# Optimization experiments

Hardware: AMD Instinct MI355X
Metric: run time of the kernel (lower is better)

## Reference

```python
import jax, jax.numpy as jnp
import numpy as np

N = 50000        # nodes
E = 100000       # directed edges
F_NODE = 22      # atom features
F_EDGE = 4       # bond features
H = 64           # hidden_dim
EPS = 1e-5       # BatchNorm eps


def setup_inputs() -> dict:
    key = jax.random.key(0)
    ks = jax.random.split(key, 16)
    s = 0.05
    return {
        "x": jax.random.normal(ks[0], (N, F_NODE), dtype=jnp.float32),
        "edge_attr": jax.random.normal(ks[1], (E, F_EDGE), dtype=jnp.float32),
        "We1": jax.random.normal(ks[2], (F_EDGE, F_NODE * H), dtype=jnp.float32) * s,
        "be1": jnp.zeros((F_NODE * H,), dtype=jnp.float32),
        "root1": jax.random.normal(ks[3], (F_NODE, H), dtype=jnp.float32) * s,
        "b1": jnp.zeros((H,), dtype=jnp.float32),
        "g1": jnp.ones((H,), dtype=jnp.float32),
        "beta1": jnp.zeros((H,), dtype=jnp.float32),
        "We2": jax.random.normal(ks[4], (F_EDGE, H * H), dtype=jnp.float32) * s,
        "be2": jnp.zeros((H * H,), dtype=jnp.float32),
        "root2": jax.random.normal(ks[5], (H, H), dtype=jnp.float32) * s,
        "b2": jnp.zeros((H,), dtype=jnp.float32),
        "g2": jnp.ones((H,), dtype=jnp.float32),
        "beta2": jnp.zeros((H,), dtype=jnp.float32),
        "Wfc": jax.random.normal(ks[6], (H, 1), dtype=jnp.float32) * s,
        "bfc": jnp.zeros((1,), dtype=jnp.float32),
        "edge_index": jax.random.randint(ks[7], (2, E), 0, N, dtype=jnp.int32),
    }


def nnconv(x, edge_index, edge_attr, We, be, root, bias, in_ch, out_ch):
    # PyG NNConv (aggr='add', root_weight=True):
    #   out_i = x_i @ root + bias + sum_{(j->i)} x_j @ reshape(MLP(e_ji), [in, out])
    src, dst = edge_index[0], edge_index[1]
    w = jax.nn.relu(edge_attr @ We + be).reshape(-1, in_ch, out_ch)  # [E, in, out]
    msg = jnp.einsum('ei,eio->eo', x[src], w)                        # [E, out]
    agg = jax.ops.segment_sum(msg, dst, num_segments=x.shape[0])     # [N, out]
    return agg + x @ root + bias


def batchnorm(x, gamma, beta):
    # training-mode BatchNorm1d: batch statistics, biased variance
    mu = jnp.mean(x, axis=0)
    var = jnp.mean(jnp.square(x - mu), axis=0)
    return (x - mu) * jax.lax.rsqrt(var + EPS) * gamma + beta


def reference(x, edge_attr, We1, be1, root1, b1, g1, beta1,
              We2, be2, root2, b2, g2, beta2, Wfc, bfc, edge_index):
    h = nnconv(x, edge_index, edge_attr, We1, be1, root1, b1, F_NODE, H)
    h = jax.nn.relu(batchnorm(h, g1, beta1))
    # dropout is identity in eval / deterministic reference
    h = nnconv(h, edge_index, edge_attr, We2, be2, root2, b2, H, H)
    h = jax.nn.relu(batchnorm(h, g2, beta2))
    return jax.nn.sigmoid(h @ Wfc + bfc)  # [N, 1]
```

## Files before the change

### kernel.cpp

```cpp
#include <hip/hip_runtime.h>
#include <math.h>

#define N_NODES 50000
#define N_EDGES 100000
#define FNODE 22
#define HDIM 64
#define BN_EPS 1e-5f

typedef __attribute__((ext_vector_type(8))) short bfrag;
typedef __attribute__((ext_vector_type(4))) float facc;
typedef __attribute__((ext_vector_type(4))) unsigned int uint4v;
typedef __attribute__((ext_vector_type(2))) unsigned int uint2v;

__device__ __forceinline__ unsigned f2bf(float x) {
    unsigned u = __float_as_uint(x);
    return (u + 0x7FFFu + ((u >> 16) & 1u)) >> 16;
}
__device__ __forceinline__ unsigned pk2bf(float lo, float hi) {
    return f2bf(lo) | (f2bf(hi) << 16);
}
__device__ __forceinline__ float bflo(unsigned w) { return __uint_as_float(w << 16); }
__device__ __forceinline__ float bfhi(unsigned w) { return __uint_as_float(w & 0xFFFF0000u); }

__global__ void k_packX(const float* __restrict__ x, unsigned* __restrict__ xbf) {
    int idx = blockIdx.x * 256 + threadIdx.x;
    if (idx < N_NODES * 12) {
        int n = idx / 12, c2 = idx - n * 12;
        int c = c2 * 2;
        float lo = (c < FNODE) ? x[n * FNODE + c] : 0.f;
        float hi = (c + 1 < FNODE) ? x[n * FNODE + c + 1] : 0.f;
        xbf[idx] = pk2bf(lo, hi);
    }
}

template <int K>
__global__ void k_packB(const float* __restrict__ W, uint4v* __restrict__ Bt) {
    constexpr int NQ = (K + 31) / 32;
    int t = threadIdx.x;
    int ot = t >> 6, lane = t & 63;
    int o = ot * 16 + (lane & 15);
    int kg = lane >> 4;
#pragma unroll
    for (int q = 0; q < NQ; ++q) {
        unsigned w[4];
#pragma unroll
        for (int p = 0; p < 4; ++p) {
            int k0 = q * 32 + kg * 8 + 2 * p;
            float lo = (k0 < K) ? W[k0 * HDIM + o] : 0.f;
            float hi = (k0 + 1 < K) ? W[(k0 + 1) * HDIM + o] : 0.f;
            w[p] = pk2bf(lo, hi);
        }
        Bt[(ot * NQ + q) * 64 + lane] = uint4v{w[0], w[1], w[2], w[3]};
    }
}

__global__ void k_node1(const float* __restrict__ x, const uint4v* __restrict__ Bt1,
                        const float* __restrict__ b1, float* __restrict__ h1) {
    int lane = threadIdx.x & 63;
    int m = lane & 15, kg = lane >> 4, orow4 = kg * 4;
    int tile = blockIdx.x * 4 + (threadIdx.x >> 6);
    int nb = tile * 16;
    if (nb >= N_NODES) return;
    const float* xr = x + (size_t)(nb + m) * FNODE;
    float xv[8];
#pragma unroll
    for (int p = 0; p < 4; ++p) {
        int c = kg * 8 + 2 * p;
        float2 v = (c + 1 < FNODE) ? *(const float2*)(xr + c) : float2{0.f, 0.f};
        xv[2 * p] = v.x; xv[2 * p + 1] = v.y;
    }
    bfrag A = __builtin_bit_cast(bfrag, uint4v{pk2bf(xv[0], xv[1]), pk2bf(xv[2], xv[3]),
                                               pk2bf(xv[4], xv[5]), pk2bf(xv[6], xv[7])});
    const facc zero4 = {0.f, 0.f, 0.f, 0.f};
#pragma unroll
    for (int ot = 0; ot < 4; ++ot) {
        bfrag B = __builtin_bit_cast(bfrag, Bt1[ot * 64 + lane]);
        facc d = __builtin_amdgcn_mfma_f32_16x16x32_bf16(A, B, zero4, 0, 0, 0);
        float bv = b1[ot * 16 + m];
#pragma unroll
        for (int j = 0; j < 4; ++j)
            h1[(size_t)(nb + orow4 + j) * HDIM + ot * 16 + m] = d[j] + bv;
    }
}

template <int IN, int ROWB, int SSTRIDE, int MINW>
__launch_bounds__(256, MINW)
__global__ void k_edge(const char* __restrict__ hrows, const float* __restrict__ ea,
                       const float* __restrict__ We, const float* __restrict__ be,
                       const int* __restrict__ eidx, float* __restrict__ out) {
    constexpr int INH = IN * HDIM;
    __shared__ uint4v Wf[IN * 32];
    __shared__ unsigned hsl[4][32 * SSTRIDE];

    int obeg = (blockIdx.x & 1) * 32;
    int tileblk = blockIdx.x >> 1;

    for (int idx = threadIdx.x; idx < IN * 32; idx += 256) {
        int i = idx >> 5, oloc = idx & 31;
        int c = i * HDIM + obeg + oloc;
        Wf[idx] = uint4v{pk2bf(We[c], We[INH + c]),
                         pk2bf(We[2 * INH + c], We[3 * INH + c]),
                         f2bf(be[c]), 0u};
    }
    __syncthreads();

    int lane = threadIdx.x & 63;
    int e16 = lane & 15;
    int orow4 = (lane >> 4) * 4;
    int tile = tileblk * 4 + (threadIdx.x >> 6);
    int ebase = tile * 32;
    if (ebase >= N_EDGES) return;
    unsigned* hs = &hsl[threadIdx.x >> 6][0];

    bool act = lane < 16;
    float4 ea0 = ((const float4*)ea)[ebase + e16];
    float4 ea1 = ((const float4*)ea)[ebase + 16 + e16];
    unsigned aone = act ? 0x3F80u : 0u;
    bfrag A0 = __builtin_bit_cast(bfrag, uint4v{act ? pk2bf(ea0.x, ea0.y) : 0u,
                                                act ? pk2bf(ea0.z, ea0.w) : 0u, aone, 0u});
    bfrag A1 = __builtin_bit_cast(bfrag, uint4v{act ? pk2bf(ea1.x, ea1.y) : 0u,
                                                act ? pk2bf(ea1.z, ea1.w) : 0u, aone, 0u});

    constexpr int SPR = ROWB / 16;
    constexpr int SLOTS = 32 * SPR;
#pragma unroll
    for (int p = 0; p < (SLOTS + 63) / 64; ++p) {
        int idx = p * 64 + lane;
        if ((SLOTS % 64 == 0) || idx < SLOTS) {
            int r = idx / SPR, c16 = idx - r * SPR;
            int src = eidx[ebase + r];
            uint4v hv = *(const uint4v*)(hrows + (size_t)src * ROWB + c16 * 16);
            *(uint4v*)&hs[r * SSTRIDE + c16 * 4] = hv;
        }
    }

    const facc zero4 = {0.f, 0.f, 0.f, 0.f};
    facc m0[2] = {zero4, zero4}, m1[2] = {zero4, zero4};

    constexpr int I4 = IN & ~3;
#pragma unroll
    for (int i0 = 0; i0 < I4; i0 += 4) {
        float hA[4][4], hB[4][4];
#pragma unroll
        for (int j = 0; j < 4; ++j) {
            uint2v wA = *(const uint2v*)&hs[(orow4 + j) * SSTRIDE + i0 / 2];
            hA[j][0] = bflo(wA.x); hA[j][1] = bfhi(wA.x);
            hA[j][2] = bflo(wA.y); hA[j][3] = bfhi(wA.y);
            uint2v wB = *(const uint2v*)&hs[(16 + orow4 + j) * SSTRIDE + i0 / 2];
            hB[j][0] = bflo(wB.x); hB[j][1] = bfhi(wB.x);
            hB[j][2] = bflo(wB.y); hB[j][3] = bfhi(wB.y);
        }
#pragma unroll
        for (int di = 0; di < 4; ++di) {
#pragma unroll
            for (int t = 0; t < 2; ++t) {
                bfrag B = __builtin_bit_cast(bfrag, Wf[(i0 + di) * 32 + t * 16 + e16]);
                facc t0 = __builtin_amdgcn_mfma_f32_16x16x32_bf16(A0, B, zero4, 0, 0, 0);
                facc t1 = __builtin_amdgcn_mfma_f32_16x16x32_bf16(A1, B, zero4, 0, 0, 0);
#pragma unroll
                for (int j = 0; j < 4; ++j) {
                    m0[t][j] = fmaf(hA[j][di], fmaxf(t0[j], 0.f), m0[t][j]);
                    m1[t][j] = fmaf(hB[j][di], fmaxf(t1[j], 0.f), m1[t][j]);
                }
            }
        }
    }
    if constexpr ((IN & 3) != 0) {
        float hA[4][2], hB[4][2];
#pragma unroll
        for (int j = 0; j < 4; ++j) {
            unsigned wA = hs[(orow4 + j) * SSTRIDE + I4 / 2];
            hA[j][0] = bflo(wA); hA[j][1] = bfhi(wA);
            unsigned wB = hs[(16 + orow4 + j) * SSTRIDE + I4 / 2];
            hB[j][0] = bflo(wB); hB[j][1] = bfhi(wB);
        }
#pragma unroll
        for (int di = 0; di < (IN & 3); ++di) {
#pragma unroll
            for (int t = 0; t < 2; ++t) {
                bfrag B = __builtin_bit_cast(bfrag, Wf[(I4 + di) * 32 + t * 16 + e16]);
                facc t0 = __builtin_amdgcn_mfma_f32_16x16x32_bf16(A0, B, zero4, 0, 0, 0);
                facc t1 = __builtin_amdgcn_mfma_f32_16x16x32_bf16(A1, B, zero4, 0, 0, 0);
#pragma unroll
                for (int j = 0; j < 4; ++j) {
                    m0[t][j] = fmaf(hA[j][di], fmaxf(t0[j], 0.f), m0[t][j]);
                    m1[t][j] = fmaf(hB[j][di], fmaxf(t1[j], 0.f), m1[t][j]);
                }
            }
        }
    }

    int dA[4], dB[4];
#pragma unroll
    for (int j = 0; j < 4; ++j) {
        dA[j] = eidx[N_EDGES + ebase + orow4 + j];
        dB[j] = eidx[N_EDGES + ebase + 16 + orow4 + j];
    }
#pragma unroll
    for (int t = 0; t < 2; ++t) {
#pragma unroll
        for (int j = 0; j < 4; ++j) {
            atomicAdd(&out[(size_t)dA[j] * HDIM + obeg + t * 16 + e16], m0[t][j]);
            atomicAdd(&out[(size_t)dB[j] * HDIM + obeg + t * 16 + e16], m1[t][j]);
        }
    }
}

__global__ void k_stats(const float* __restrict__ hbuf, float* stats) {
    int c = threadIdx.x & 63;
    int r = threadIdx.x >> 6;
    int rowsPer = blockDim.x >> 6;
    float s = 0.f, q = 0.f;
    for (int n = blockIdx.x * rowsPer + r; n < N_NODES; n += gridDim.x * rowsPer) {
        float v = hbuf[n * HDIM + c];
        s += v;
        q = fmaf(v, v, q);
    }
    __shared__ float ls[4][64], lq[4][64];
    ls[r][c] = s;
    lq[r][c] = q;
    __syncthreads();
    if (r == 0) {
        s = ls[0][c] + ls[1][c] + ls[2][c] + ls[3][c];
        q = lq[0][c] + lq[1][c] + lq[2][c] + lq[3][c];
        atomicAdd(&stats[c], s);
        atomicAdd(&stats[64 + c], q);
    }
}

__global__ void k_finalize(const float* stats_in, const float* __restrict__ g,
                           const float* __restrict__ beta, float* as_out) {
    int c = threadIdx.x;
    float mu = stats_in[c] * (1.f / N_NODES);
    float var = stats_in[64 + c] * (1.f / N_NODES) - mu * mu;
    var = fmaxf(var, 0.f);
    float a = g[c] * rsqrtf(var + BN_EPS);
    as_out[c] = a;
    as_out[64 + c] = beta[c] - mu * a;
}

__global__ void k_apply1(const float* h1, const float* __restrict__ as1,
                         const uint4v* __restrict__ Bt, const float* __restrict__ b2,
                         unsigned* __restrict__ hbf, float* h2) {
    int lane = threadIdx.x & 63;
    int m = lane & 15, kg = lane >> 4, orow4 = (lane >> 4) * 4;
    int tile = blockIdx.x * 4 + (threadIdx.x >> 6);
    int nb = tile * 16;
    if (nb >= N_NODES) return;
    int node = nb + m;
    const float* hr = h1 + (size_t)node * HDIM;

    float4 a0 = *(const float4*)(as1 + kg * 8), a1 = *(const float4*)(as1 + kg * 8 + 4);
    float4 s0 = *(const float4*)(as1 + 64 + kg * 8), s1 = *(const float4*)(as1 + 64 + kg * 8 + 4);
    float4 a2 = *(const float4*)(as1 + 32 + kg * 8), a3 = *(const float4*)(as1 + 32 + kg * 8 + 4);
    float4 s2 = *(const float4*)(as1 + 96 + kg * 8), s3 = *(const float4*)(as1 + 96 + kg * 8 + 4);

    float4 v0 = *(const float4*)(hr + kg * 8), v1 = *(const float4*)(hr + kg * 8 + 4);
    float4 v2 = *(const float4*)(hr + 32 + kg * 8), v3 = *(const float4*)(hr + 32 + kg * 8 + 4);

    float r0[8], r1[8];
#pragma unroll
    for (int p = 0; p < 4; ++p) {
        r0[p]     = fmaxf(fmaf((&v0.x)[p], (&a0.x)[p], (&s0.x)[p]), 0.f);
        r0[p + 4] = fmaxf(fmaf((&v1.x)[p], (&a1.x)[p], (&s1.x)[p]), 0.f);
        r1[p]     = fmaxf(fmaf((&v2.x)[p], (&a2.x)[p], (&s2.x)[p]), 0.f);
        r1[p + 4] = fmaxf(fmaf((&v3.x)[p], (&a3.x)[p], (&s3.x)[p]), 0.f);
    }
    uint4v pk0 = uint4v{pk2bf(r0[0], r0[1]), pk2bf(r0[2], r0[3]),
                        pk2bf(r0[4], r0[5]), pk2bf(r0[6], r0[7])};
    uint4v pk1 = uint4v{pk2bf(r1[0], r1[1]), pk2bf(r1[2], r1[3]),
                        pk2bf(r1[4], r1[5]), pk2bf(r1[6], r1[7])};
    *(uint4v*)(hbf + (size_t)node * 32 + kg * 4)      = pk0;
    *(uint4v*)(hbf + (size_t)node * 32 + 16 + kg * 4) = pk1;

    bfrag A0 = __builtin_bit_cast(bfrag, pk0);
    bfrag A1 = __builtin_bit_cast(bfrag, pk1);

    const facc zero4 = {0.f, 0.f, 0.f, 0.f};
#pragma unroll
    for (int ot = 0; ot < 4; ++ot) {
        bfrag B0 = __builtin_bit_cast(bfrag, Bt[(ot * 2 + 0) * 64 + lane]);
        bfrag B1 = __builtin_bit_cast(bfrag, Bt[(ot * 2 + 1) * 64 + lane]);
        facc d = __builtin_amdgcn_mfma_f32_16x16x32_bf16(A0, B0, zero4, 0, 0, 0);
        d = __builtin_amdgcn_mfma_f32_16x16x32_bf16(A1, B1, d, 0, 0, 0);
        float bv = b2[ot * 16 + m];
#pragma unroll
        for (int j = 0; j < 4; ++j)
            h2[(size_t)(nb + orow4 + j) * HDIM + ot * 16 + m] = d[j] + bv;
    }
}

__global__ void k_final(const float* __restrict__ h2, const float* __restrict__ as2,
                        const float* __restrict__ Wfc, const float* __restrict__ bfc,
                        float* __restrict__ out) {
    int lane = threadIdx.x & 63;
    int n = blockIdx.x * (blockDim.x >> 6) + (threadIdx.x >> 6);
    if (n >= N_NODES) return;
    float a = as2[lane], s = as2[64 + lane];
    float v = fmaxf(fmaf(h2[n * HDIM + lane], a, s), 0.f) * Wfc[lane];
#pragma unroll
    for (int off = 32; off > 0; off >>= 1) v += __shfl_xor(v, off, 64);
    if (lane == 0) out[n] = 1.f / (1.f + expf(-(v + bfc[0])));
}

extern "C" void kernel_launch(void* const* d_in, const int* in_sizes, int n_in,
                              void* d_out, int out_size, void* d_ws, size_t ws_size,
                              hipStream_t stream) {
    const float* x     = (const float*)d_in[0];
    const float* ea    = (const float*)d_in[1];
    const float* We1   = (const float*)d_in[2];
    const float* be1   = (const float*)d_in[3];
    const float* root1 = (const float*)d_in[4];
    const float* b1    = (const float*)d_in[5];
    const float* g1    = (const float*)d_in[6];
    const float* beta1 = (const float*)d_in[7];
    const float* We2   = (const float*)d_in[8];
    const float* be2   = (const float*)d_in[9];
    const float* root2 = (const float*)d_in[10];
    const float* b2    = (const float*)d_in[11];
    const float* g2    = (const float*)d_in[12];
    const float* beta2 = (const float*)d_in[13];
    const float* Wfc   = (const float*)d_in[14];
    const float* bfc   = (const float*)d_in[15];
    const int*   eidx  = (const int*)d_in[16];
    float* out = (float*)d_out;

    char* ws = (char*)d_ws;
    size_t off = 0;
    auto alloc = [&](size_t bytes) { char* p = ws + off; off = (off + bytes + 255) & ~(size_t)255; return p; };
    float*    h1    = (float*)alloc((size_t)N_NODES * HDIM * 4);
    unsigned* hbf   = (unsigned*)alloc((size_t)N_NODES * 32 * 4);
    unsigned* xbf   = (unsigned*)alloc((size_t)N_NODES * 12 * 4);
    float*    stats = (float*)alloc(512 * 4);
    uint4v*   Bt2   = (uint4v*)alloc(8 * 64 * 16);
    uint4v*   Bt1   = (uint4v*)alloc(4 * 64 * 16);

    hipMemsetAsync(stats, 0, 512 * sizeof(float), stream);
    k_packX<<<(N_NODES * 12 + 255) / 256, 256, 0, stream>>>(x, xbf);
    k_packB<HDIM><<<1, 256, 0, stream>>>(root2, Bt2);
    k_packB<FNODE><<<1, 256, 0, stream>>>(root1, Bt1);

    const int edgeBlocks = 2 * ((N_EDGES / 32 + 3) / 4);
    const int nodeBlocks = (N_NODES + 3) / 4;
    const int tileBlocks = (N_NODES / 16 + 3) / 4;

    k_node1<<<tileBlocks, 256, 0, stream>>>(x, Bt1, b1, h1);
    k_edge<FNODE, 48, 20, 4><<<edgeBlocks, 256, 0, stream>>>((const char*)xbf, ea,
                                                             We1, be1, eidx, h1);
    k_stats<<<256, 256, 0, stream>>>(h1, stats);
    k_finalize<<<1, 64, 0, stream>>>(stats, g1, beta1, stats + 128);
    k_apply1<<<tileBlocks, 256, 0, stream>>>(h1, stats + 128, Bt2, b2, hbf, h1);
    k_edge<HDIM, 128, 36, 3><<<edgeBlocks, 256, 0, stream>>>((const char*)hbf, ea,
                                                             We2, be2, eidx, h1);
    k_stats<<<256, 256, 0, stream>>>(h1, stats + 256);
    k_finalize<<<1, 64, 0, stream>>>(stats + 256, g2, beta2, stats + 384);
    k_final<<<nodeBlocks, 256, 0, stream>>>(h1, stats + 384, Wfc, bfc, out);
}
```

Measured before the change: 174.8 us.

## Specialize layer-1 edge kernel to 16-edge tiles covering all 64 outputs

Splits the templated edge kernel into two specialized kernels. The layer-1 kernel now has each wave handle 16 edges across all 64 output channels, with no split of output halves across blocks. It stages the gathered source features as fp32 in shared memory, so the inner loop uses vector float4 reads instead of bf16 unpacking. This avoids the redundant gather and edge-attribute load per output half, at the cost of a larger shared weight table per block. The layer-2 kernel is the same code with its template constants hard-wired.

After: 173.1 us. Within noise of the previous version (-1.0%).

```diff
diff --git a/kernel.cpp b/kernel.cpp
--- a/kernel.cpp
+++ b/kernel.cpp
@@ -83,12 +83,106 @@
     }
 }
 
-template <int IN, int ROWB, int SSTRIDE, int MINW>
-__launch_bounds__(256, MINW)
-__global__ void k_edge(const char* __restrict__ hrows, const float* __restrict__ ea,
-                       const float* __restrict__ We, const float* __restrict__ be,
-                       const int* __restrict__ eidx, float* __restrict__ out) {
+__launch_bounds__(256, 4)
+__global__ void k_edge1(const char* __restrict__ hrows, const float* __restrict__ ea,
+                        const float* __restrict__ We, const float* __restrict__ be,
+                        const int* __restrict__ eidx, float* __restrict__ out) {
+    constexpr int IN = FNODE;
     constexpr int INH = IN * HDIM;
+    __shared__ uint4v Wf[IN * HDIM];
+    __shared__ float hsl[4][16 * 28];
+
+    for (int idx = threadIdx.x; idx < IN * HDIM; idx += 256) {
+        int i = idx >> 6, o = idx & 63;
+        int c = i * HDIM + o;
+        Wf[idx] = uint4v{pk2bf(We[c], We[INH + c]),
+                         pk2bf(We[2 * INH + c], We[3 * INH + c]),
+                         f2bf(be[c]), 0u};
+    }
+    __syncthreads();
+
+    int lane = threadIdx.x & 63;
+    int e16 = lane & 15;
+    int orow4 = (lane >> 4) * 4;
+    int tile = blockIdx.x * 4 + (threadIdx.x >> 6);
+    int ebase = tile * 16;
+    if (ebase >= N_EDGES) return;
+    float* hs = &hsl[threadIdx.x >> 6][0];
+
+    bool act = lane < 16;
+    float4 ea0 = ((const float4*)ea)[ebase + e16];
+    unsigned aone = act ? 0x3F80u : 0u;
+    bfrag A0 = __builtin_bit_cast(bfrag, uint4v{act ? pk2bf(ea0.x, ea0.y) : 0u,
+                                                act ? pk2bf(ea0.z, ea0.w) : 0u, aone, 0u});
+
+    if (lane < 48) {
+        int r = lane / 3, c16 = lane - r * 3;
+        int src = eidx[ebase + r];
+        uint4v hv = *(const uint4v*)(hrows + (size_t)src * 48 + c16 * 16);
+        *(float4*)&hs[r * 28 + c16 * 8] =
+            float4{bflo(hv.x), bfhi(hv.x), bflo(hv.y), bfhi(hv.y)};
+        *(float4*)&hs[r * 28 + c16 * 8 + 4] =
+            float4{bflo(hv.z), bfhi(hv.z), bflo(hv.w), bfhi(hv.w)};
+    }
+
+    const facc zero4 = {0.f, 0.f, 0.f, 0.f};
+    facc m0[4] = {zero4, zero4, zero4, zero4};
+
+#pragma unroll
+    for (int i0 = 0; i0 < 20; i0 += 4) {
+        float4 hA[4];
+#pragma unroll
+        for (int j = 0; j < 4; ++j)
+            hA[j] = *(const float4*)&hs[(orow4 + j) * 28 + i0];
+#pragma unroll
+        for (int di = 0; di < 4; ++di) {
+#pragma unroll
+            for (int t = 0; t < 4; ++t) {
+                bfrag B = __builtin_bit_cast(bfrag, Wf[(i0 + di) * 64 + t * 16 + e16]);
+                facc t0 = __builtin_amdgcn_mfma_f32_16x16x32_bf16(A0, B, zero4, 0, 0, 0);
+#pragma unroll
+                for (int j = 0; j < 4; ++j)
+                    m0[t][j] = fmaf((&hA[j].x)[di], fmaxf(t0[j], 0.f), m0[t][j]);
+            }
+        }
+    }
+    {
+        float4 hA[4];
+#pragma unroll
+        for (int j = 0; j < 4; ++j)
+            hA[j] = *(const float4*)&hs[(orow4 + j) * 28 + 20];
+#pragma unroll
+        for (int di = 0; di < 2; ++di) {
+#pragma unroll
+            for (int t = 0; t < 4; ++t) {
+                bfrag B = __builtin_bit_cast(bfrag, Wf[(20 + di) * 64 + t * 16 + e16]);
+                facc t0 = __builtin_amdgcn_mfma_f32_16x16x32_bf16(A0, B, zero4, 0, 0, 0);
+#pragma unroll
+                for (int j = 0; j < 4; ++j)
+                    m0[t][j] = fmaf((&hA[j].x)[di], fmaxf(t0[j], 0.f), m0[t][j]);
+            }
+        }
+    }
+
+    int dA[4];
+#pragma unroll
+    for (int j = 0; j < 4; ++j)
+        dA[j] = eidx[N_EDGES + ebase + orow4 + j];
+#pragma unroll
+    for (int t = 0; t < 4; ++t) {
+#pragma unroll
+        for (int j = 0; j < 4; ++j)
+            atomicAdd(&out[(size_t)dA[j] * HDIM + t * 16 + e16], m0[t][j]);
+    }
+}
+
+__launch_bounds__(256, 3)
+__global__ void k_edge2(const char* __restrict__ hrows, const float* __restrict__ ea,
+                        const float* __restrict__ We, const float* __restrict__ be,
+                        const int* __restrict__ eidx, float* __restrict__ out) {
+    constexpr int IN = HDIM;
+    constexpr int INH = IN * HDIM;
+    constexpr int SSTRIDE = 36;
     __shared__ uint4v Wf[IN * 32];
     __shared__ unsigned hsl[4][32 * SSTRIDE];
 
@@ -121,25 +215,20 @@
     bfrag A1 = __builtin_bit_cast(bfrag, uint4v{act ? pk2bf(ea1.x, ea1.y) : 0u,
                                                 act ? pk2bf(ea1.z, ea1.w) : 0u, aone, 0u});
 
-    constexpr int SPR = ROWB / 16;
-    constexpr int SLOTS = 32 * SPR;
-#pragma unroll
-    for (int p = 0; p < (SLOTS + 63) / 64; ++p) {
+#pragma unroll
+    for (int p = 0; p < 4; ++p) {
         int idx = p * 64 + lane;
-        if ((SLOTS % 64 == 0) || idx < SLOTS) {
-            int r = idx / SPR, c16 = idx - r * SPR;
-            int src = eidx[ebase + r];
-            uint4v hv = *(const uint4v*)(hrows + (size_t)src * ROWB + c16 * 16);
-            *(uint4v*)&hs[r * SSTRIDE + c16 * 4] = hv;
-        }
+        int r = idx >> 3, c16 = idx & 7;
+        int src = eidx[ebase + r];
+        uint4v hv = *(const uint4v*)(hrows + (size_t)src * 128 + c16 * 16);
+        *(uint4v*)&hs[r * SSTRIDE + c16 * 4] = hv;
     }
 
     const facc zero4 = {0.f, 0.f, 0.f, 0.f};
     facc m0[2] = {zero4, zero4}, m1[2] = {zero4, zero4};
 
-    constexpr int I4 = IN & ~3;
-#pragma unroll
-    for (int i0 = 0; i0 < I4; i0 += 4) {
+#pragma unroll
+    for (int i0 = 0; i0 < IN; i0 += 4) {
         float hA[4][4], hB[4][4];
 #pragma unroll
         for (int j = 0; j < 4; ++j) {
@@ -155,30 +244,6 @@
 #pragma unroll
             for (int t = 0; t < 2; ++t) {
                 bfrag B = __builtin_bit_cast(bfrag, Wf[(i0 + di) * 32 + t * 16 + e16]);
-                facc t0 = __builtin_amdgcn_mfma_f32_16x16x32_bf16(A0, B, zero4, 0, 0, 0);
-                facc t1 = __builtin_amdgcn_mfma_f32_16x16x32_bf16(A1, B, zero4, 0, 0, 0);
-#pragma unroll
-                for (int j = 0; j < 4; ++j) {
-                    m0[t][j] = fmaf(hA[j][di], fmaxf(t0[j], 0.f), m0[t][j]);
-                    m1[t][j] = fmaf(hB[j][di], fmaxf(t1[j], 0.f), m1[t][j]);
-                }
-            }
-        }
-    }
-    if constexpr ((IN & 3) != 0) {
-        float hA[4][2], hB[4][2];
-#pragma unroll
-        for (int j = 0; j < 4; ++j) {
-            unsigned wA = hs[(orow4 + j) * SSTRIDE + I4 / 2];
-            hA[j][0] = bflo(wA); hA[j][1] = bfhi(wA);
-            unsigned wB = hs[(16 + orow4 + j) * SSTRIDE + I4 / 2];
-            hB[j][0] = bflo(wB); hB[j][1] = bfhi(wB);
-        }
-#pragma unroll
-        for (int di = 0; di < (IN & 3); ++di) {
-#pragma unroll
-            for (int t = 0; t < 2; ++t) {
-                bfrag B = __builtin_bit_cast(bfrag, Wf[(I4 + di) * 32 + t * 16 + e16]);
                 facc t0 = __builtin_amdgcn_mfma_f32_16x16x32_bf16(A0, B, zero4, 0, 0, 0);
                 facc t1 = __builtin_amdgcn_mfma_f32_16x16x32_bf16(A1, B, zero4, 0, 0, 0);
 #pragma unroll
@@ -340,18 +405,17 @@
     k_packB<HDIM><<<1, 256, 0, stream>>>(root2, Bt2);
     k_packB<FNODE><<<1, 256, 0, stream>>>(root1, Bt1);
 
-    const int edgeBlocks = 2 * ((N_EDGES / 32 + 3) / 4);
+    const int e1Blocks = (N_EDGES / 16 + 3) / 4;
+    const int e2Blocks = 2 * ((N_EDGES / 32 + 3) / 4);
     const int nodeBlocks = (N_NODES + 3) / 4;
     const int tileBlocks = (N_NODES / 16 + 3) / 4;
 
     k_node1<<<tileBlocks, 256, 0, stream>>>(x, Bt1, b1, h1);
-    k_edge<FNODE, 48, 20, 4><<<edgeBlocks, 256, 0, stream>>>((const char*)xbf, ea,
-                                                             We1, be1, eidx, h1);
+    k_edge1<<<e1Blocks, 256, 0, stream>>>((const char*)xbf, ea, We1, be1, eidx, h1);
     k_stats<<<256, 256, 0, stream>>>(h1, stats);
     k_finalize<<<1, 64, 0, stream>>>(stats, g1, beta1, stats + 128);
     k_apply1<<<tileBlocks, 256, 0, stream>>>(h1, stats + 128, Bt2, b2, hbf, h1);
-    k_edge<HDIM, 128, 36, 3><<<edgeBlocks, 256, 0, stream>>>((const char*)hbf, ea,
-                                                             We2, be2, eidx, h1);
+    k_edge2<<<e2Blocks, 256, 0, stream>>>((const char*)hbf, ea, We2, be2, eidx, h1);
     k_stats<<<256, 256, 0, stream>>>(h1, stats + 256);
     k_finalize<<<1, 64, 0, stream>>>(stats + 256, g2, beta2, stats + 384);
     k_final<<<nodeBlocks, 256, 0, stream>>>(h1, stats + 384, Wfc, bfc, out);
```
